# Optimization experiments

Measured on AMD Instinct MI355X. Metric: run time of the kernel, lower is better.

## Reference

```python
import jax, jax.numpy as jnp
import numpy as np
import math

H = 16  # num heads
NEG = -1e9


def setup_inputs() -> dict:
    key = jax.random.key(0)
    ks = jax.random.split(key, 12)
    B, S, D = 2, 2048, 1024
    inp = {
        "query": jax.random.normal(ks[0], (B, S, D), jnp.float32),
        "key": jax.random.normal(ks[1], (B, S, D), jnp.float32),
        "value": jax.random.normal(ks[2], (B, S, D), jnp.float32),
        "mask": jax.random.randint(ks[3], (B, 1, S), 0, 2, jnp.int32),
        "wq": jax.random.normal(ks[4], (D, D), jnp.float32) * 0.02,
        "bq": jnp.zeros((D,), jnp.float32),
        "wk": jax.random.normal(ks[5], (D, D), jnp.float32) * 0.02,
        "bk": jnp.zeros((D,), jnp.float32),
        "wv": jax.random.normal(ks[6], (D, D), jnp.float32) * 0.02,
        "bv": jnp.zeros((D,), jnp.float32),
        "wo": jax.random.normal(ks[7], (D, D), jnp.float32) * 0.02,
        "bo": jnp.zeros((D,), jnp.float32),
    }
    return inp


def reference(query, key, value, mask, wq, bq, wk, bk, wv, bv, wo, bo):
    B, S, D = query.shape
    dk = D // H

    def proj(x, w, b):
        # torch Linear: x @ w.T + b ; then split heads -> [B, H, S, dk]
        y = x @ w.T + b
        return y.reshape(B, -1, H, dk).transpose(0, 2, 1, 3)

    q = proj(query, wq, bq)
    k = proj(key, wk, bk)
    v = proj(value, wv, bv)

    scores = jnp.einsum("bhqd,bhkd->bhqk", q, k) / math.sqrt(dk)  # [B,H,S,S]

    m = mask[:, None, :, :]  # [B,1,1,S] (mask.unsqueeze(1) in torch)
    scores = jnp.where(m == 0, NEG, scores)            # key-side padding mask
    scores = jnp.where(jnp.swapaxes(m, -2, -1) == 0, NEG, scores)  # query-side mask (q_len>1)

    p_attn = jax.nn.softmax(scores, axis=-1)
    # dropout p=0 / eval mode -> identity
    ctx = jnp.einsum("bhqk,bhkd->bhqd", p_attn, v)  # [B,H,S,dk]
    ctx = ctx.transpose(0, 2, 1, 3).reshape(B, S, H * dk)
    out = ctx @ wo.T + bo
    return out
```

## Files before the change

kernel.cpp:

```cpp
#include <hip/hip_runtime.h>
#include <hip/hip_bf16.h>

#define SEQ 2048
#define DIM 1024
#define NH  16
#define DK  64
#define NA  (2 * SEQ * DIM)
#define NW  (DIM * DIM)
#define PSTR 72
#define QSCALE 0.18033688011112042f

typedef __attribute__((ext_vector_type(4))) float f32x4;
typedef __attribute__((ext_vector_type(8))) __bf16 bf16x8;
typedef __attribute__((ext_vector_type(4))) __bf16 bf16x4;

__device__ __forceinline__ f32x4 mfma16(bf16x8 a, bf16x8 b, f32x4 c) {
  return __builtin_amdgcn_mfma_f32_16x16x32_bf16(a, b, c, 0, 0, 0);
}
__device__ __forceinline__ void async_load16(const void* g, void* l) {
  __builtin_amdgcn_global_load_lds(
      (const __attribute__((address_space(1))) void*)g,
      (__attribute__((address_space(3))) void*)l, 16, 0, 0);
}
__device__ __forceinline__ int swz(int row, int chunk) {
  return row * 8 + (chunk ^ (row & 7));
}

__global__ __launch_bounds__(256) void cvt_kernel(
    const float* __restrict__ s0, const float* __restrict__ s1,
    const float* __restrict__ s2, const float* __restrict__ s3,
    const float* __restrict__ s4, const float* __restrict__ s5,
    const float* __restrict__ s6,
    __hip_bfloat16* __restrict__ d0, __hip_bfloat16* __restrict__ d1,
    __hip_bfloat16* __restrict__ d2, __hip_bfloat16* __restrict__ d3,
    __hip_bfloat16* __restrict__ d4, __hip_bfloat16* __restrict__ d5,
    __hip_bfloat16* __restrict__ d6) {
  const int t = blockIdx.y;
  const float* s;
  __hip_bfloat16* d;
  int n;
  switch (t) {
    case 0: s = s0; d = d0; n = NA; break;
    case 1: s = s1; d = d1; n = NA; break;
    case 2: s = s2; d = d2; n = NA; break;
    case 3: s = s3; d = d3; n = NW; break;
    case 4: s = s4; d = d4; n = NW; break;
    case 5: s = s5; d = d5; n = NW; break;
    default: s = s6; d = d6; n = NW; break;
  }
  size_t i = ((size_t)blockIdx.x * 256 + threadIdx.x) * 8;
  if (i >= (size_t)n) return;
  float4 a = *(const float4*)(s + i);
  float4 b = *(const float4*)(s + i + 4);
  bf16x8 v = {(__bf16)a.x, (__bf16)a.y, (__bf16)a.z, (__bf16)a.w,
              (__bf16)b.x, (__bf16)b.y, (__bf16)b.z, (__bf16)b.w};
  *(bf16x8*)(d + i) = v;
}

__device__ __forceinline__ void gemm_mainloop(
    const __hip_bfloat16* __restrict__ X, const __hip_bfloat16* __restrict__ W,
    __hip_bfloat16* A_lds, __hip_bfloat16* B_lds, int m0, int n0,
    f32x4 acc[4][4]) {
  const int K = DIM;
  const int tid = threadIdx.x, lane = tid & 63, w = tid >> 6;
  const int quad = lane >> 4, l15 = lane & 15;
  const int wm = (w >> 1) * 64, wn = (w & 1) * 64;

  f32x4 z = {0.f, 0.f, 0.f, 0.f};
  for (int mi = 0; mi < 4; ++mi)
    for (int ni = 0; ni < 4; ++ni) acc[mi][ni] = z;

  for (int k0 = 0; k0 < K; k0 += 64) {
    for (int r = 0; r < 4; ++r) {
      int cbase = r * 256 + w * 64;
      int c = cbase + lane, row = c >> 3, cs = c & 7;
      int off = cs ^ (row & 7);
      async_load16((const char*)(X + (size_t)(m0 + row) * K + k0) + off * 16,
                   (char*)A_lds + cbase * 16);
      async_load16((const char*)(W + (size_t)(n0 + row) * K + k0) + off * 16,
                   (char*)B_lds + cbase * 16);
    }
    __syncthreads();
    for (int kk = 0; kk < 2; ++kk) {
      bf16x8 a[4], b[4];
      for (int mi = 0; mi < 4; ++mi)
        a[mi] = *(const bf16x8*)(A_lds + swz(wm + mi * 16 + l15, kk * 4 + quad) * 8);
      for (int ni = 0; ni < 4; ++ni)
        b[ni] = *(const bf16x8*)(B_lds + swz(wn + ni * 16 + l15, kk * 4 + quad) * 8);
      for (int mi = 0; mi < 4; ++mi)
        for (int ni = 0; ni < 4; ++ni)
          acc[mi][ni] = mfma16(a[mi], b[ni], acc[mi][ni]);
    }
    __syncthreads();
  }
}

__global__ __launch_bounds__(256) void qkv_proj_kernel(
    const __hip_bfloat16* __restrict__ xq, const __hip_bfloat16* __restrict__ xk,
    const __hip_bfloat16* __restrict__ xv,
    const __hip_bfloat16* __restrict__ wq, const __hip_bfloat16* __restrict__ wk,
    const __hip_bfloat16* __restrict__ wv,
    const float* __restrict__ bq, const float* __restrict__ bk,
    const float* __restrict__ bv,
    __hip_bfloat16* __restrict__ q_ws, __hip_bfloat16* __restrict__ k_ws,
    __hip_bfloat16* __restrict__ vt_ws) {
  __shared__ __align__(16) __hip_bfloat16 A_lds[128 * 64];
  __shared__ __align__(16) __hip_bfloat16 B_lds[128 * 64];

  const int z = blockIdx.z;
  const __hip_bfloat16* X = (z == 0) ? xq : ((z == 1) ? xk : xv);
  const __hip_bfloat16* W = (z == 0) ? wq : ((z == 1) ? wk : wv);
  const float* bias = (z == 0) ? bq : ((z == 1) ? bk : bv);
  __hip_bfloat16* out = (z == 0) ? q_ws : ((z == 1) ? k_ws : vt_ws);
  const float f = (z == 0) ? QSCALE : 1.0f;

  const int m0 = blockIdx.y * 128, n0 = blockIdx.x * 128;
  f32x4 acc[4][4];
  gemm_mainloop(X, W, A_lds, B_lds, m0, n0, acc);

  const int tid = threadIdx.x, lane = tid & 63, w = tid >> 6;
  const int quad = lane >> 4, l15 = lane & 15;
  const int wm = (w >> 1) * 64, wn = (w & 1) * 64;

  for (int mi = 0; mi < 4; ++mi)
    for (int ni = 0; ni < 4; ++ni) {
      const int n = n0 + wn + ni * 16 + l15;
      const float bv_ = bias[n];
      const int h = n >> 6, d = n & 63;
      for (int r = 0; r < 4; ++r) {
        const int m = m0 + wm + mi * 16 + quad * 4 + r;
        const int b = m >> 11, s = m & 2047;
        const float v = (acc[mi][ni][r] + bv_) * f;
        size_t addr;
        if (z == 2)
          addr = ((size_t)(b * NH + h) * DK + d) * SEQ + s;
        else
          addr = ((size_t)(b * NH + h) * SEQ + s) * DK + d;
        out[addr] = __float2bfloat16(v);
      }
    }
}

__global__ __launch_bounds__(256) void attn_kernel(
    const __hip_bfloat16* __restrict__ qg, const __hip_bfloat16* __restrict__ kg,
    const __hip_bfloat16* __restrict__ vtg, const int* __restrict__ mask,
    __hip_bfloat16* __restrict__ ctx) {
  __shared__ __align__(16) __hip_bfloat16 QP_lds[128 * PSTR];
  __shared__ __align__(16) __hip_bfloat16 K_lds[64 * 64];
  __shared__ __align__(16) __hip_bfloat16 V_lds[64 * 64];
  __shared__ float bias_lds[SEQ];

  const int tid = threadIdx.x, lane = tid & 63, w = tid >> 6;
  const int quad = lane >> 4, l15 = lane & 15;
  const int bh = blockIdx.y, b = bh >> 4, h = bh & 15;
  const int q0 = blockIdx.x * 128;
  const size_t head = (size_t)bh * SEQ * DK;

  for (int i = tid; i < SEQ; i += 256)
    bias_lds[i] = mask[b * SEQ + i] ? 0.f : -1e9f;

  for (int r = 0; r < 4; ++r) {
    int cbase = r * 256 + w * 64;
    int c = cbase + lane, row = c >> 3, cs = c & 7;
    int off = cs ^ (row & 7);
    async_load16((const char*)(qg + head + (size_t)(q0 + row) * DK) + off * 16,
                 (char*)QP_lds + cbase * 16);
  }
  __syncthreads();

  bf16x8 qf[2][2];
  for (int kk = 0; kk < 2; ++kk)
    for (int ni = 0; ni < 2; ++ni)
      qf[kk][ni] = *(const bf16x8*)(QP_lds + swz(w * 32 + ni * 16 + l15, kk * 4 + quad) * 8);

  int qmv[2];
  for (int ni = 0; ni < 2; ++ni)
    qmv[ni] = mask[b * SEQ + q0 + w * 32 + ni * 16 + l15];

  __hip_bfloat16* P_lds = QP_lds;

  f32x4 z = {0.f, 0.f, 0.f, 0.f};
  f32x4 o_acc[2][4];
  for (int ni = 0; ni < 2; ++ni)
    for (int di = 0; di < 4; ++di) o_acc[ni][di] = z;
  float lsum[2] = {0.f, 0.f};

  for (int t = 0; t < 32; ++t) {
    const int k0 = t * 64;
    for (int r = 0; r < 2; ++r) {
      int cbase = r * 256 + w * 64;
      int c = cbase + lane, row = c >> 3, cs = c & 7;
      int off = cs ^ (row & 7);
      async_load16((const char*)(kg + head + (size_t)(k0 + row) * DK) + off * 16,
                   (char*)K_lds + cbase * 16);
      async_load16(
          (const char*)(vtg + (size_t)bh * DK * SEQ + (size_t)row * SEQ + k0) + off * 16,
          (char*)V_lds + cbase * 16);
    }
    __syncthreads();

    f32x4 s_acc[4][2];
    for (int mi = 0; mi < 4; ++mi)
      for (int ni = 0; ni < 2; ++ni) s_acc[mi][ni] = z;
    for (int kk = 0; kk < 2; ++kk) {
      bf16x8 ak[4];
      for (int mi = 0; mi < 4; ++mi)
        ak[mi] = *(const bf16x8*)(K_lds + swz(mi * 16 + l15, kk * 4 + quad) * 8);
      for (int mi = 0; mi < 4; ++mi)
        for (int ni = 0; ni < 2; ++ni)
          s_acc[mi][ni] = mfma16(ak[mi], qf[kk][ni], s_acc[mi][ni]);
    }

    for (int mi = 0; mi < 4; ++mi) {
      f32x4 kb = *(const f32x4*)(bias_lds + k0 + mi * 16 + quad * 4);
      for (int ni = 0; ni < 2; ++ni) {
        bf16x4 pk;
        for (int r = 0; r < 4; ++r) {
          float s2 = s_acc[mi][ni][r] + kb[r];
          s2 = qmv[ni] ? s2 : 0.f;
          float p = __builtin_amdgcn_exp2f(s2);
          lsum[ni] += p;
          pk[r] = (__bf16)p;
        }
        *(bf16x4*)(P_lds + (w * 32 + ni * 16 + l15) * PSTR + mi * 16 + quad * 4) = pk;
      }
    }

    for (int kk = 0; kk < 2; ++kk) {
      bf16x8 av[4], bp[2];
      for (int di = 0; di < 4; ++di)
        av[di] = *(const bf16x8*)(V_lds + swz(di * 16 + l15, kk * 4 + quad) * 8);
      for (int ni = 0; ni < 2; ++ni)
        bp[ni] = *(const bf16x8*)(P_lds + (w * 32 + ni * 16 + l15) * PSTR + kk * 32 + quad * 8);
      for (int ni = 0; ni < 2; ++ni)
        for (int di = 0; di < 4; ++di)
          o_acc[ni][di] = mfma16(av[di], bp[ni], o_acc[ni][di]);
    }
    __syncthreads();
  }

  for (int ni = 0; ni < 2; ++ni) {
    lsum[ni] += __shfl_xor(lsum[ni], 16);
    lsum[ni] += __shfl_xor(lsum[ni], 32);
  }
  const float inv[2] = {1.f / lsum[0], 1.f / lsum[1]};

  for (int ni = 0; ni < 2; ++ni)
    for (int di = 0; di < 4; ++di) {
      bf16x4 ov;
      for (int r = 0; r < 4; ++r) ov[r] = (__bf16)(o_acc[ni][di][r] * inv[ni]);
      *(bf16x4*)(P_lds + (w * 32 + ni * 16 + l15) * PSTR + di * 16 + quad * 4) = ov;
    }
  __syncthreads();
  for (int r = 0; r < 4; ++r) {
    int c = r * 256 + tid, row = c >> 3, off = c & 7;
    *(uint4*)(ctx + (size_t)(b * SEQ + q0 + row) * DIM + h * DK + off * 8) =
        *(const uint4*)(P_lds + row * PSTR + off * 8);
  }
}

__global__ __launch_bounds__(256) void out_proj_kernel(
    const __hip_bfloat16* __restrict__ ctx, const __hip_bfloat16* __restrict__ wo,
    const float* __restrict__ bo, float* __restrict__ out) {
  __shared__ __align__(16) __hip_bfloat16 A_lds[128 * 64];
  __shared__ __align__(16) __hip_bfloat16 B_lds[128 * 64];

  const int m0 = blockIdx.y * 128, n0 = blockIdx.x * 128;
  f32x4 acc[4][4];
  gemm_mainloop(ctx, wo, A_lds, B_lds, m0, n0, acc);

  const int tid = threadIdx.x, lane = tid & 63, w = tid >> 6;
  const int quad = lane >> 4, l15 = lane & 15;
  const int wm = (w >> 1) * 64, wn = (w & 1) * 64;

  for (int mi = 0; mi < 4; ++mi)
    for (int ni = 0; ni < 4; ++ni) {
      const int n = n0 + wn + ni * 16 + l15;
      const float bv_ = bo[n];
      for (int r = 0; r < 4; ++r) {
        const int m = m0 + wm + mi * 16 + quad * 4 + r;
        out[(size_t)m * DIM + n] = acc[mi][ni][r] + bv_;
      }
    }
}

extern "C" void kernel_launch(void* const* d_in, const int* in_sizes, int n_in,
                              void* d_out, int out_size, void* d_ws, size_t ws_size,
                              hipStream_t stream) {
  const float* query = (const float*)d_in[0];
  const float* key   = (const float*)d_in[1];
  const float* value = (const float*)d_in[2];
  const int*   mask  = (const int*)d_in[3];
  const float* wq = (const float*)d_in[4];
  const float* bq = (const float*)d_in[5];
  const float* wk = (const float*)d_in[6];
  const float* bk = (const float*)d_in[7];
  const float* wv = (const float*)d_in[8];
  const float* bv = (const float*)d_in[9];
  const float* wo = (const float*)d_in[10];
  const float* bo = (const float*)d_in[11];
  float* out = (float*)d_out;

  char* ws = (char*)d_ws;
  const size_t SZA = (size_t)NA * 2;
  const size_t SZW = (size_t)NW * 2;
  __hip_bfloat16* xq  = (__hip_bfloat16*)(ws);
  __hip_bfloat16* xk  = (__hip_bfloat16*)(ws + SZA);
  __hip_bfloat16* xv  = (__hip_bfloat16*)(ws + 2 * SZA);
  __hip_bfloat16* wqb = (__hip_bfloat16*)(ws + 3 * SZA);
  __hip_bfloat16* wkb = (__hip_bfloat16*)(ws + 3 * SZA + SZW);
  __hip_bfloat16* wvb = (__hip_bfloat16*)(ws + 3 * SZA + 2 * SZW);
  __hip_bfloat16* wob = (__hip_bfloat16*)(ws + 3 * SZA + 3 * SZW);
  __hip_bfloat16* q_ws  = (__hip_bfloat16*)(ws + 3 * SZA + 4 * SZW);
  __hip_bfloat16* k_ws  = (__hip_bfloat16*)(ws + 4 * SZA + 4 * SZW);
  __hip_bfloat16* vt_ws = (__hip_bfloat16*)(ws + 5 * SZA + 4 * SZW);
  __hip_bfloat16* ctx_ws = xq;

  dim3 blk(256);
  cvt_kernel<<<dim3(2048, 7), blk, 0, stream>>>(
      query, key, value, wq, wk, wv, wo, xq, xk, xv, wqb, wkb, wvb, wob);
  qkv_proj_kernel<<<dim3(8, 32, 3), blk, 0, stream>>>(
      xq, xk, xv, wqb, wkb, wvb, bq, bk, bv, q_ws, k_ws, vt_ws);
  attn_kernel<<<dim3(16, 32), blk, 0, stream>>>(q_ws, k_ws, vt_ws, mask, ctx_ws);
  out_proj_kernel<<<dim3(8, 32), blk, 0, stream>>>(ctx_ws, wob, bo, out);
}
```

Before: 263.3 us.

## Stage V-transpose through LDS, widen attention to 8 waves, compute row sums via MFMA

The QKV projection now writes the transposed V tile through a padded LDS buffer, so global stores are coalesced 16-byte vectors instead of scattered 2-byte ones. The attention kernel moves from 256 to 512 threads, with each wave owning 16 query rows instead of 32, which halves per-wave register use and raises wave parallelism. The key mask bias is folded into the MFMA accumulator init. Softmax row sums come from an extra MFMA against a vector of ones instead of scalar adds and shuffles. The costs are an extra MFMA per step, more block-wide synchronisation per tile, and row sums accumulated from bf16-rounded probabilities.

```diff
diff --git a/kernel.cpp b/kernel.cpp
--- a/kernel.cpp
+++ b/kernel.cpp
@@ -8,6 +8,7 @@
 #define NA  (2 * SEQ * DIM)
 #define NW  (DIM * DIM)
 #define PSTR 72
+#define TSTR 132
 #define QSCALE 0.18033688011112042f
 
 typedef __attribute__((ext_vector_type(4))) float f32x4;
@@ -104,44 +105,58 @@
     const float* __restrict__ bv,
     __hip_bfloat16* __restrict__ q_ws, __hip_bfloat16* __restrict__ k_ws,
     __hip_bfloat16* __restrict__ vt_ws) {
-  __shared__ __align__(16) __hip_bfloat16 A_lds[128 * 64];
-  __shared__ __align__(16) __hip_bfloat16 B_lds[128 * 64];
+  __shared__ __align__(16) __hip_bfloat16 S_lds[128 * TSTR];
 
   const int z = blockIdx.z;
   const __hip_bfloat16* X = (z == 0) ? xq : ((z == 1) ? xk : xv);
   const __hip_bfloat16* W = (z == 0) ? wq : ((z == 1) ? wk : wv);
   const float* bias = (z == 0) ? bq : ((z == 1) ? bk : bv);
-  __hip_bfloat16* out = (z == 0) ? q_ws : ((z == 1) ? k_ws : vt_ws);
   const float f = (z == 0) ? QSCALE : 1.0f;
 
   const int m0 = blockIdx.y * 128, n0 = blockIdx.x * 128;
   f32x4 acc[4][4];
-  gemm_mainloop(X, W, A_lds, B_lds, m0, n0, acc);
+  gemm_mainloop(X, W, S_lds, S_lds + 128 * 64, m0, n0, acc);
 
   const int tid = threadIdx.x, lane = tid & 63, w = tid >> 6;
   const int quad = lane >> 4, l15 = lane & 15;
   const int wm = (w >> 1) * 64, wn = (w & 1) * 64;
 
-  for (int mi = 0; mi < 4; ++mi)
-    for (int ni = 0; ni < 4; ++ni) {
-      const int n = n0 + wn + ni * 16 + l15;
-      const float bv_ = bias[n];
-      const int h = n >> 6, d = n & 63;
-      for (int r = 0; r < 4; ++r) {
-        const int m = m0 + wm + mi * 16 + quad * 4 + r;
-        const int b = m >> 11, s = m & 2047;
-        const float v = (acc[mi][ni][r] + bv_) * f;
-        size_t addr;
-        if (z == 2)
-          addr = ((size_t)(b * NH + h) * DK + d) * SEQ + s;
-        else
-          addr = ((size_t)(b * NH + h) * SEQ + s) * DK + d;
-        out[addr] = __float2bfloat16(v);
+  if (z != 2) {
+    __hip_bfloat16* out = (z == 0) ? q_ws : k_ws;
+    for (int mi = 0; mi < 4; ++mi)
+      for (int ni = 0; ni < 4; ++ni) {
+        const int n = n0 + wn + ni * 16 + l15;
+        const float bv_ = bias[n];
+        const int h = n >> 6, d = n & 63;
+        for (int r = 0; r < 4; ++r) {
+          const int m = m0 + wm + mi * 16 + quad * 4 + r;
+          const int b = m >> 11, s = m & 2047;
+          out[((size_t)(b * NH + h) * SEQ + s) * DK + d] =
+              __float2bfloat16((acc[mi][ni][r] + bv_) * f);
+        }
       }
-    }
-}
-
-__global__ __launch_bounds__(256) void attn_kernel(
+  } else {
+    for (int mi = 0; mi < 4; ++mi)
+      for (int ni = 0; ni < 4; ++ni) {
+        const int n_local = wn + ni * 16 + l15;
+        const float bv_ = bias[n0 + n_local];
+        bf16x4 tv;
+        for (int r = 0; r < 4; ++r) tv[r] = (__bf16)(acc[mi][ni][r] + bv_);
+        *(bf16x4*)(S_lds + n_local * TSTR + wm + mi * 16 + quad * 4) = tv;
+      }
+    __syncthreads();
+    const int b = m0 >> 11, s_base = m0 & 2047;
+    for (int r2 = 0; r2 < 8; ++r2) {
+      int c2 = r2 * 256 + tid;
+      int nrow = c2 >> 4, moff = (c2 & 15) * 8;
+      int n = n0 + nrow, h = n >> 6, d = n & 63;
+      *(uint4*)(vt_ws + ((size_t)(b * NH + h) * DK + d) * SEQ + s_base + moff) =
+          *(const uint4*)(S_lds + nrow * TSTR + moff);
+    }
+  }
+}
+
+__global__ __launch_bounds__(512) void attn_kernel(
     const __hip_bfloat16* __restrict__ qg, const __hip_bfloat16* __restrict__ kg,
     const __hip_bfloat16* __restrict__ vtg, const int* __restrict__ mask,
     __hip_bfloat16* __restrict__ ctx) {
@@ -156,11 +171,11 @@
   const int q0 = blockIdx.x * 128;
   const size_t head = (size_t)bh * SEQ * DK;
 
-  for (int i = tid; i < SEQ; i += 256)
+  for (int i = tid; i < SEQ; i += 512)
     bias_lds[i] = mask[b * SEQ + i] ? 0.f : -1e9f;
 
-  for (int r = 0; r < 4; ++r) {
-    int cbase = r * 256 + w * 64;
+  for (int r = 0; r < 2; ++r) {
+    int cbase = r * 512 + w * 64;
     int c = cbase + lane, row = c >> 3, cs = c & 7;
     int off = cs ^ (row & 7);
     async_load16((const char*)(qg + head + (size_t)(q0 + row) * DK) + off * 16,
@@ -168,92 +183,75 @@
   }
   __syncthreads();
 
-  bf16x8 qf[2][2];
+  bf16x8 qf[2];
   for (int kk = 0; kk < 2; ++kk)
-    for (int ni = 0; ni < 2; ++ni)
-      qf[kk][ni] = *(const bf16x8*)(QP_lds + swz(w * 32 + ni * 16 + l15, kk * 4 + quad) * 8);
-
-  int qmv[2];
-  for (int ni = 0; ni < 2; ++ni)
-    qmv[ni] = mask[b * SEQ + q0 + w * 32 + ni * 16 + l15];
+    qf[kk] = *(const bf16x8*)(QP_lds + swz(w * 16 + l15, kk * 4 + quad) * 8);
+  const int qmv = mask[b * SEQ + q0 + w * 16 + l15];
 
   __hip_bfloat16* P_lds = QP_lds;
+  const bf16x8 ones = {(__bf16)1.f, (__bf16)1.f, (__bf16)1.f, (__bf16)1.f,
+                       (__bf16)1.f, (__bf16)1.f, (__bf16)1.f, (__bf16)1.f};
 
   f32x4 z = {0.f, 0.f, 0.f, 0.f};
-  f32x4 o_acc[2][4];
-  for (int ni = 0; ni < 2; ++ni)
-    for (int di = 0; di < 4; ++di) o_acc[ni][di] = z;
-  float lsum[2] = {0.f, 0.f};
+  f32x4 o_acc[4];
+  for (int di = 0; di < 4; ++di) o_acc[di] = z;
+  f32x4 o_sum = z;
 
   for (int t = 0; t < 32; ++t) {
     const int k0 = t * 64;
-    for (int r = 0; r < 2; ++r) {
-      int cbase = r * 256 + w * 64;
-      int c = cbase + lane, row = c >> 3, cs = c & 7;
+    {
+      int c = tid, row = c >> 3, cs = c & 7;
       int off = cs ^ (row & 7);
       async_load16((const char*)(kg + head + (size_t)(k0 + row) * DK) + off * 16,
-                   (char*)K_lds + cbase * 16);
+                   (char*)K_lds + c * 16);
       async_load16(
           (const char*)(vtg + (size_t)bh * DK * SEQ + (size_t)row * SEQ + k0) + off * 16,
-          (char*)V_lds + cbase * 16);
-    }
-    __syncthreads();
-
-    f32x4 s_acc[4][2];
+          (char*)V_lds + c * 16);
+    }
+    __syncthreads();
+
+    f32x4 s_acc[4];
     for (int mi = 0; mi < 4; ++mi)
-      for (int ni = 0; ni < 2; ++ni) s_acc[mi][ni] = z;
+      s_acc[mi] = *(const f32x4*)(bias_lds + k0 + mi * 16 + quad * 4);
     for (int kk = 0; kk < 2; ++kk) {
       bf16x8 ak[4];
       for (int mi = 0; mi < 4; ++mi)
         ak[mi] = *(const bf16x8*)(K_lds + swz(mi * 16 + l15, kk * 4 + quad) * 8);
       for (int mi = 0; mi < 4; ++mi)
-        for (int ni = 0; ni < 2; ++ni)
-          s_acc[mi][ni] = mfma16(ak[mi], qf[kk][ni], s_acc[mi][ni]);
+        s_acc[mi] = mfma16(ak[mi], qf[kk], s_acc[mi]);
     }
 
     for (int mi = 0; mi < 4; ++mi) {
-      f32x4 kb = *(const f32x4*)(bias_lds + k0 + mi * 16 + quad * 4);
-      for (int ni = 0; ni < 2; ++ni) {
-        bf16x4 pk;
-        for (int r = 0; r < 4; ++r) {
-          float s2 = s_acc[mi][ni][r] + kb[r];
-          s2 = qmv[ni] ? s2 : 0.f;
-          float p = __builtin_amdgcn_exp2f(s2);
-          lsum[ni] += p;
-          pk[r] = (__bf16)p;
-        }
-        *(bf16x4*)(P_lds + (w * 32 + ni * 16 + l15) * PSTR + mi * 16 + quad * 4) = pk;
+      bf16x4 pk;
+      for (int r = 0; r < 4; ++r) {
+        float s2 = qmv ? s_acc[mi][r] : 0.f;
+        pk[r] = (__bf16)__builtin_amdgcn_exp2f(s2);
       }
+      *(bf16x4*)(P_lds + (w * 16 + l15) * PSTR + mi * 16 + quad * 4) = pk;
     }
 
     for (int kk = 0; kk < 2; ++kk) {
-      bf16x8 av[4], bp[2];
+      bf16x8 bp = *(const bf16x8*)(P_lds + (w * 16 + l15) * PSTR + kk * 32 + quad * 8);
+      bf16x8 av[4];
       for (int di = 0; di < 4; ++di)
         av[di] = *(const bf16x8*)(V_lds + swz(di * 16 + l15, kk * 4 + quad) * 8);
-      for (int ni = 0; ni < 2; ++ni)
-        bp[ni] = *(const bf16x8*)(P_lds + (w * 32 + ni * 16 + l15) * PSTR + kk * 32 + quad * 8);
-      for (int ni = 0; ni < 2; ++ni)
-        for (int di = 0; di < 4; ++di)
-          o_acc[ni][di] = mfma16(av[di], bp[ni], o_acc[ni][di]);
-    }
-    __syncthreads();
-  }
-
-  for (int ni = 0; ni < 2; ++ni) {
-    lsum[ni] += __shfl_xor(lsum[ni], 16);
-    lsum[ni] += __shfl_xor(lsum[ni], 32);
-  }
-  const float inv[2] = {1.f / lsum[0], 1.f / lsum[1]};
-
-  for (int ni = 0; ni < 2; ++ni)
-    for (int di = 0; di < 4; ++di) {
-      bf16x4 ov;
-      for (int r = 0; r < 4; ++r) ov[r] = (__bf16)(o_acc[ni][di][r] * inv[ni]);
-      *(bf16x4*)(P_lds + (w * 32 + ni * 16 + l15) * PSTR + di * 16 + quad * 4) = ov;
-    }
+      for (int di = 0; di < 4; ++di)
+        o_acc[di] = mfma16(av[di], bp, o_acc[di]);
+      o_sum = mfma16(ones, bp, o_sum);
+    }
+    __syncthreads();
+  }
+
+  const float inv = 1.f / o_sum[0];
+
+  for (int di = 0; di < 4; ++di) {
+    bf16x4 ov;
+    for (int r = 0; r < 4; ++r) ov[r] = (__bf16)(o_acc[di][r] * inv);
+    *(bf16x4*)(P_lds + (w * 16 + l15) * PSTR + di * 16 + quad * 4) = ov;
+  }
   __syncthreads();
-  for (int r = 0; r < 4; ++r) {
-    int c = r * 256 + tid, row = c >> 3, off = c & 7;
+  for (int r = 0; r < 2; ++r) {
+    int c = r * 512 + tid, row = c >> 3, off = c & 7;
     *(uint4*)(ctx + (size_t)(b * SEQ + q0 + row) * DIM + h * DK + off * 8) =
         *(const uint4*)(P_lds + row * PSTR + off * 8);
   }
@@ -316,11 +314,10 @@
   __hip_bfloat16* vt_ws = (__hip_bfloat16*)(ws + 5 * SZA + 4 * SZW);
   __hip_bfloat16* ctx_ws = xq;
 
-  dim3 blk(256);
-  cvt_kernel<<<dim3(2048, 7), blk, 0, stream>>>(
+  cvt_kernel<<<dim3(2048, 7), dim3(256), 0, stream>>>(
       query, key, value, wq, wk, wv, wo, xq, xk, xv, wqb, wkb, wvb, wob);
-  qkv_proj_kernel<<<dim3(8, 32, 3), blk, 0, stream>>>(
+  qkv_proj_kernel<<<dim3(8, 32, 3), dim3(256), 0, stream>>>(
       xq, xk, xv, wqb, wkb, wvb, bq, bk, bv, q_ws, k_ws, vt_ws);
-  attn_kernel<<<dim3(16, 32), blk, 0, stream>>>(q_ws, k_ws, vt_ws, mask, ctx_ws);
-  out_proj_kernel<<<dim3(8, 32), blk, 0, stream>>>(ctx_ws, wob, bo, out);
-}
+  attn_kernel<<<dim3(16, 32), dim3(512), 0, stream>>>(q_ws, k_ws, vt_ws, mask, ctx_ws);
+  out_proj_kernel<<<dim3(8, 32), dim3(256), 0, stream>>>(ctx_ws, wob, bo, out);
+}
```

New measurement: 239.6 us. 9.0% less time.
